# Optimization experiments

Measured on AMD Instinct MI355X. Metric: run time of the kernel, lower is better.

Reference implementation:

```python
import jax, jax.numpy as jnp
import numpy as np

B, D, G, H = 65536, 512, 16, 128


def setup_inputs() -> dict:
    key = jax.random.key(0)
    ks = jax.random.split(key, 8)
    s = 1.0 / np.sqrt(D)
    sh = 1.0 / np.sqrt(H)
    return {
        "z": jax.random.normal(ks[0], (B, D), dtype=jnp.float32),
        "Wc": jax.random.uniform(ks[1], (D, G), jnp.float32, -s, s),
        "bc": jax.random.uniform(ks[2], (G,), jnp.float32, -s, s),
        "W1": jax.random.uniform(ks[3], (G, D, H), jnp.float32, -s, s),
        "b1": jax.random.uniform(ks[4], (G, H), jnp.float32, -s, s),
        "W2": jax.random.uniform(ks[5], (G, H), jnp.float32, -sh, sh),
        "b2": jax.random.uniform(ks[6], (G,), jnp.float32, -sh, sh),
    }


def reference(z, Wc, bc, W1, b1, W2, b2):
    # classifier head + softmax
    logits = z @ Wc + bc                                  # [B, G]
    p_g = jax.nn.softmax(logits, axis=1)                  # [B, G]
    # G experts fused as one batched GEMM: fc1 -> GELU -> fc2 (dropout = identity at eval)
    h = jax.nn.gelu(jnp.einsum('bd,gdh->bgh', z, W1) + b1, approximate=False)  # [B, G, H]
    y_all = jnp.einsum('bgh,gh->bg', h, W2) + b2          # [B, G]
    return logits, p_g, y_all
```

## Files before the change

### kernel.cpp

```cpp
#include <hip/hip_runtime.h>
#include <cstdint>
#include <cstddef>

typedef __bf16 bf16x8 __attribute__((ext_vector_type(8)));
typedef float f32x4 __attribute__((ext_vector_type(4)));
typedef unsigned short ushortx8 __attribute__((ext_vector_type(8)));

__device__ __forceinline__ unsigned short f2bf(float f) {
  union { float f; unsigned int u; } v; v.f = f;
  return (unsigned short)((v.u + 0x8000u) >> 16);
}

__device__ __forceinline__ float gelu_s(float x) {
  float x2 = x * x;
  float p = __builtin_fmaf(x2, -0.10294324f, -2.30220819f);
  float e = __builtin_amdgcn_exp2f(x * p);
  return x * __builtin_amdgcn_rcpf(1.0f + e);
}

#define GLOAD16(gsrc, ldst)                                                  \
  __builtin_amdgcn_global_load_lds(                                          \
      (const __attribute__((address_space(1))) unsigned int*)(gsrc),         \
      (__attribute__((address_space(3))) unsigned int*)(uintptr_t)(          \
          (char*)(ldst)),                                                    \
      16, 0, 0)

#define SWZ_FRAG(base, R, C8)                                                \
  (*(const bf16x8*)((base) + (((R) >> 5) * 4096) +                           \
                    ((((R)&31) * 8 + ((C8) ^ ((R)&7))) * 16)))

__global__ __launch_bounds__(256) void k_convert(
    const float* __restrict__ z, const float* __restrict__ W1,
    const float* __restrict__ Wc, unsigned short* __restrict__ zb,
    unsigned short* __restrict__ w1t, unsigned short* __restrict__ wct) {
  int bid = blockIdx.x;
  int tid = threadIdx.x;
  if (bid < 16384) {
    size_t i = ((size_t)bid * 256 + tid) * 8;
    const float4* p = (const float4*)(z + i);
    float4 a = p[0], b = p[1];
    ushortx8 r;
    r[0] = f2bf(a.x); r[1] = f2bf(a.y); r[2] = f2bf(a.z); r[3] = f2bf(a.w);
    r[4] = f2bf(b.x); r[5] = f2bf(b.y); r[6] = f2bf(b.z); r[7] = f2bf(b.w);
    *(ushortx8*)(zb + i) = r;
  } else if (bid < 16384 + 1024) {
    __shared__ float tile[32][33];
    int b = bid - 16384;
    int gg = b >> 6;
    int t = b & 63;
    int d0 = (t >> 2) * 32;
    int h0 = (t & 3) * 32;
    int tx = tid & 31, ty = tid >> 5;
#pragma unroll
    for (int r = 0; r < 4; ++r) {
      int d = d0 + r * 8 + ty;
      tile[r * 8 + ty][tx] = W1[(gg << 16) + d * 128 + h0 + tx];
    }
    __syncthreads();
#pragma unroll
    for (int r = 0; r < 4; ++r) {
      int h = h0 + r * 8 + ty;
      w1t[(gg << 16) + h * 512 + d0 + tx] = f2bf(tile[tx][r * 8 + ty]);
    }
  } else {
#pragma unroll
    for (int j = 0; j < 32; ++j) {
      int i = j * 256 + tid;
      wct[(i & 15) * 512 + (i >> 4)] = f2bf(Wc[i]);
    }
  }
}

__global__ __launch_bounds__(256, 3) void k_main(
    const unsigned short* __restrict__ zb,
    const unsigned short* __restrict__ w1t,
    const unsigned short* __restrict__ wct,
    const float* __restrict__ bc, const float* __restrict__ b1,
    const float* __restrict__ w2, const float* __restrict__ b2,
    float* __restrict__ out) {
  __shared__ alignas(16) char lds[8192 + 32768 + 1024];
  const int tid = threadIdx.x;
  const int wq = tid >> 6;
  const int ln = tid & 63;
  const int l15 = ln & 15;
  const int l4 = ln >> 4;
  const int c8s = (((tid & 7) ^ ((tid >> 3) & 7))) * 8;
  char* ldsB = lds + 8192;

  if (blockIdx.x >= 512) {
    const int eb = blockIdx.x - 512;
    const int p = eb >> 10;
    const int mbase = (eb & 1023) * 64;
    const unsigned short* ag = zb + (size_t)(mbase + (tid >> 3)) * 512 + c8s;
    const unsigned short* bg = w1t + p * 131072 + (tid >> 3) * 512 + c8s;
    const int e = p * 2 + (wq >> 1);
    const int nb = (wq & 1) * 64;
    f32x4 acc[4][4] = {};
    for (int kt = 0; kt < 8; ++kt) {
      const int ko = kt * 64;
#pragma unroll
      for (int it = 0; it < 2; ++it)
        GLOAD16(ag + it * 32 * 512 + ko, lds + it * 4096 + tid * 16);
#pragma unroll
      for (int it = 0; it < 8; ++it)
        GLOAD16(bg + it * 32 * 512 + ko, ldsB + it * 4096 + tid * 16);
      __syncthreads();
#pragma unroll
      for (int ks = 0; ks < 2; ++ks) {
        bf16x8 af[4];
#pragma unroll
        for (int rt = 0; rt < 4; ++rt)
          af[rt] = SWZ_FRAG(lds, rt * 16 + l15, ks * 4 + l4);
#pragma unroll
        for (int ct = 0; ct < 4; ++ct) {
          bf16x8 bf = SWZ_FRAG(ldsB, wq * 64 + ct * 16 + l15, ks * 4 + l4);
#pragma unroll
          for (int rt = 0; rt < 4; ++rt)
            acc[rt][ct] = __builtin_amdgcn_mfma_f32_16x16x32_bf16(
                af[rt], bf, acc[rt][ct], 0, 0, 0);
        }
      }
      __syncthreads();
    }
    float b1v[4], w2v[4];
#pragma unroll
    for (int ct = 0; ct < 4; ++ct) {
      int n = nb + ct * 16 + l15;
      b1v[ct] = b1[e * 128 + n];
      w2v[ct] = w2[e * 128 + n];
    }
    float* ylds = (float*)(lds + 40960);
#pragma unroll
    for (int rt = 0; rt < 4; ++rt) {
#pragma unroll
      for (int i = 0; i < 4; ++i) {
        float s = 0.0f;
#pragma unroll
        for (int ct = 0; ct < 4; ++ct)
          s += gelu_s(acc[rt][ct][i] + b1v[ct]) * w2v[ct];
#pragma unroll
        for (int off = 1; off < 16; off <<= 1)
          s += __shfl_xor(s, off, 16);
        if (l15 == 0) ylds[wq * 64 + rt * 16 + l4 * 4 + i] = s;
      }
    }
    __syncthreads();
    if (tid < 128) {
      int row = tid & 63, ee = tid >> 6;
      float y = ylds[ee * 128 + row] + ylds[ee * 128 + 64 + row] +
                b2[p * 2 + ee];
      out[(size_t)2097152 + (size_t)(mbase + row) * 16 + p * 2 + ee] = y;
    }
  } else {
    const int mbase = blockIdx.x * 128;
    const unsigned short* ag = zb + (size_t)(mbase + (tid >> 3)) * 512 + c8s;
    const unsigned short* wb = wct + l15 * 512 + l4 * 8;
    f32x4 acc2[2] = {};
    for (int kt = 0; kt < 8; ++kt) {
      const int ko = kt * 64;
#pragma unroll
      for (int it = 0; it < 4; ++it)
        GLOAD16(ag + it * 32 * 512 + ko, lds + it * 4096 + tid * 16);
      bf16x8 bfr0 = *(const bf16x8*)(wb + ko);
      bf16x8 bfr1 = *(const bf16x8*)(wb + ko + 32);
      __syncthreads();
#pragma unroll
      for (int rt = 0; rt < 2; ++rt) {
        bf16x8 a0 = SWZ_FRAG(lds, wq * 32 + rt * 16 + l15, l4);
        acc2[rt] = __builtin_amdgcn_mfma_f32_16x16x32_bf16(a0, bfr0, acc2[rt],
                                                           0, 0, 0);
        bf16x8 a1 = SWZ_FRAG(lds, wq * 32 + rt * 16 + l15, 4 + l4);
        acc2[rt] = __builtin_amdgcn_mfma_f32_16x16x32_bf16(a1, bfr1, acc2[rt],
                                                           0, 0, 0);
      }
      __syncthreads();
    }
    float bcv = bc[l15];
#pragma unroll
    for (int rt = 0; rt < 2; ++rt) {
#pragma unroll
      for (int i = 0; i < 4; ++i) {
        int row = wq * 32 + rt * 16 + l4 * 4 + i;
        float lg = acc2[rt][i] + bcv;
        float mx = lg;
#pragma unroll
        for (int off = 1; off < 16; off <<= 1)
          mx = fmaxf(mx, __shfl_xor(mx, off, 16));
        float ex = __expf(lg - mx);
        float sm = ex;
#pragma unroll
        for (int off = 1; off < 16; off <<= 1)
          sm += __shfl_xor(sm, off, 16);
        size_t ro = (size_t)(mbase + row) * 16 + l15;
        out[ro] = lg;
        out[1048576 + ro] = ex / sm;
      }
    }
  }
}

extern "C" void kernel_launch(void* const* d_in, const int* in_sizes, int n_in,
                              void* d_out, int out_size, void* d_ws,
                              size_t ws_size, hipStream_t stream) {
  const float* z = (const float*)d_in[0];
  const float* Wc = (const float*)d_in[1];
  const float* bc = (const float*)d_in[2];
  const float* W1 = (const float*)d_in[3];
  const float* b1 = (const float*)d_in[4];
  const float* W2 = (const float*)d_in[5];
  const float* b2 = (const float*)d_in[6];
  float* out = (float*)d_out;

  unsigned short* zb = (unsigned short*)d_ws;
  unsigned short* w1t = zb + (size_t)65536 * 512;
  unsigned short* wct = w1t + (size_t)16 * 128 * 512;

  k_convert<<<16384 + 1024 + 1, 256, 0, stream>>>(z, W1, Wc, zb, w1t, wct);
  k_main<<<512 + 8 * 1024, 256, 0, stream>>>(zb, w1t, wct, bc, b1, W2, b2,
                                             out);
}
```

Baseline: 400.5 us.

## Retile expert GEMM to 128x128 per single expert with block remapping

The expert GEMM tile changes from 64 rows by two experts (64x256) to 128 rows by one expert (128x128), arranged as 2x2 waves. This shrinks the LDS footprint so launch bounds can ask for four blocks per CU, and balances A and B loads per K step. Block indices are remapped so that neighbouring blocks share the same rows across experts, which should improve L2 reuse of z. The bf16 conversion also switches to four float4 iterations per thread, using half as many blocks. In exchange, each block now reads z rows once per expert instead of once per expert pair.

```diff
diff --git a/kernel.cpp b/kernel.cpp
--- a/kernel.cpp
+++ b/kernel.cpp
@@ -5,6 +5,7 @@
 typedef __bf16 bf16x8 __attribute__((ext_vector_type(8)));
 typedef float f32x4 __attribute__((ext_vector_type(4)));
 typedef unsigned short ushortx8 __attribute__((ext_vector_type(8)));
+typedef unsigned short ushortx4 __attribute__((ext_vector_type(4)));
 
 __device__ __forceinline__ unsigned short f2bf(float f) {
   union { float f; unsigned int u; } v; v.f = f;
@@ -35,17 +36,20 @@
     unsigned short* __restrict__ w1t, unsigned short* __restrict__ wct) {
   int bid = blockIdx.x;
   int tid = threadIdx.x;
-  if (bid < 16384) {
-    size_t i = ((size_t)bid * 256 + tid) * 8;
-    const float4* p = (const float4*)(z + i);
-    float4 a = p[0], b = p[1];
-    ushortx8 r;
-    r[0] = f2bf(a.x); r[1] = f2bf(a.y); r[2] = f2bf(a.z); r[3] = f2bf(a.w);
-    r[4] = f2bf(b.x); r[5] = f2bf(b.y); r[6] = f2bf(b.z); r[7] = f2bf(b.w);
-    *(ushortx8*)(zb + i) = r;
-  } else if (bid < 16384 + 1024) {
+  if (bid < 8192) {
+    const float4* z4 = (const float4*)z;
+    size_t base = (size_t)bid * 1024 + tid;
+#pragma unroll
+    for (int it = 0; it < 4; ++it) {
+      size_t i4 = base + (size_t)it * 256;
+      float4 a = z4[i4];
+      ushortx4 r;
+      r[0] = f2bf(a.x); r[1] = f2bf(a.y); r[2] = f2bf(a.z); r[3] = f2bf(a.w);
+      *(ushortx4*)(zb + i4 * 4) = r;
+    }
+  } else if (bid < 8192 + 1024) {
     __shared__ float tile[32][33];
-    int b = bid - 16384;
+    int b = bid - 8192;
     int gg = b >> 6;
     int t = b & 63;
     int d0 = (t >> 2) * 32;
@@ -71,38 +75,40 @@
   }
 }
 
-__global__ __launch_bounds__(256, 3) void k_main(
+__global__ __launch_bounds__(256, 4) void k_main(
     const unsigned short* __restrict__ zb,
     const unsigned short* __restrict__ w1t,
     const unsigned short* __restrict__ wct,
     const float* __restrict__ bc, const float* __restrict__ b1,
     const float* __restrict__ w2, const float* __restrict__ b2,
     float* __restrict__ out) {
-  __shared__ alignas(16) char lds[8192 + 32768 + 1024];
+  __shared__ alignas(16) char lds[16384 + 16384 + 1024];
   const int tid = threadIdx.x;
   const int wq = tid >> 6;
   const int ln = tid & 63;
   const int l15 = ln & 15;
   const int l4 = ln >> 4;
   const int c8s = (((tid & 7) ^ ((tid >> 3) & 7))) * 8;
-  char* ldsB = lds + 8192;
+  char* ldsB = lds + 16384;
 
   if (blockIdx.x >= 512) {
     const int eb = blockIdx.x - 512;
-    const int p = eb >> 10;
-    const int mbase = (eb & 1023) * 64;
+    const int idx = (eb & 7) * 1024 + (eb >> 3);
+    const int e = idx & 15;
+    const int mbase = (idx >> 4) * 128;
     const unsigned short* ag = zb + (size_t)(mbase + (tid >> 3)) * 512 + c8s;
-    const unsigned short* bg = w1t + p * 131072 + (tid >> 3) * 512 + c8s;
-    const int e = p * 2 + (wq >> 1);
-    const int nb = (wq & 1) * 64;
+    const unsigned short* bg =
+        w1t + e * 65536 + (tid >> 3) * 512 + c8s;
+    const int wr = wq >> 1;
+    const int wc = wq & 1;
     f32x4 acc[4][4] = {};
     for (int kt = 0; kt < 8; ++kt) {
       const int ko = kt * 64;
 #pragma unroll
-      for (int it = 0; it < 2; ++it)
+      for (int it = 0; it < 4; ++it)
         GLOAD16(ag + it * 32 * 512 + ko, lds + it * 4096 + tid * 16);
 #pragma unroll
-      for (int it = 0; it < 8; ++it)
+      for (int it = 0; it < 4; ++it)
         GLOAD16(bg + it * 32 * 512 + ko, ldsB + it * 4096 + tid * 16);
       __syncthreads();
 #pragma unroll
@@ -110,14 +116,14 @@
         bf16x8 af[4];
 #pragma unroll
         for (int rt = 0; rt < 4; ++rt)
-          af[rt] = SWZ_FRAG(lds, rt * 16 + l15, ks * 4 + l4);
+          af[rt] = SWZ_FRAG(lds, wr * 64 + rt * 16 + l15, ks * 4 + l4);
 #pragma unroll
         for (int ct = 0; ct < 4; ++ct) {
-          bf16x8 bf = SWZ_FRAG(ldsB, wq * 64 + ct * 16 + l15, ks * 4 + l4);
+          bf16x8 bfv = SWZ_FRAG(ldsB, wc * 64 + ct * 16 + l15, ks * 4 + l4);
 #pragma unroll
           for (int rt = 0; rt < 4; ++rt)
             acc[rt][ct] = __builtin_amdgcn_mfma_f32_16x16x32_bf16(
-                af[rt], bf, acc[rt][ct], 0, 0, 0);
+                af[rt], bfv, acc[rt][ct], 0, 0, 0);
         }
       }
       __syncthreads();
@@ -125,11 +131,11 @@
     float b1v[4], w2v[4];
 #pragma unroll
     for (int ct = 0; ct < 4; ++ct) {
-      int n = nb + ct * 16 + l15;
+      int n = wc * 64 + ct * 16 + l15;
       b1v[ct] = b1[e * 128 + n];
       w2v[ct] = w2[e * 128 + n];
     }
-    float* ylds = (float*)(lds + 40960);
+    float* ylds = (float*)(lds + 32768);
 #pragma unroll
     for (int rt = 0; rt < 4; ++rt) {
 #pragma unroll
@@ -146,10 +152,9 @@
     }
     __syncthreads();
     if (tid < 128) {
-      int row = tid & 63, ee = tid >> 6;
-      float y = ylds[ee * 128 + row] + ylds[ee * 128 + 64 + row] +
-                b2[p * 2 + ee];
-      out[(size_t)2097152 + (size_t)(mbase + row) * 16 + p * 2 + ee] = y;
+      int rl = tid & 63, half = tid >> 6;
+      float y = ylds[half * 128 + rl] + ylds[half * 128 + 64 + rl] + b2[e];
+      out[(size_t)2097152 + (size_t)(mbase + half * 64 + rl) * 16 + e] = y;
     }
   } else {
     const int mbase = blockIdx.x * 128;
@@ -215,7 +220,6 @@
   unsigned short* w1t = zb + (size_t)65536 * 512;
   unsigned short* wct = w1t + (size_t)16 * 128 * 512;
 
-  k_convert<<<16384 + 1024 + 1, 256, 0, stream>>>(z, W1, Wc, zb, w1t, wct);
-  k_main<<<512 + 8 * 1024, 256, 0, stream>>>(zb, w1t, wct, bc, b1, W2, b2,
-                                             out);
-}
+  k_convert<<<8192 + 1024 + 1, 256, 0, stream>>>(z, W1, Wc, zb, w1t, wct);
+  k_main<<<512 + 8192, 256, 0, stream>>>(zb, w1t, wct, bc, b1, W2, b2, out);
+}
```

New measurement: 375.6 us. -6.2%, faster.
